# Optimization experiments

Measured on AMD Instinct MI355X. Metric: run time of the kernel, lower is better.

The kernel has to match this reference:

```python
import jax, jax.numpy as jnp
import numpy as np

N = 50000   # nodes of the target node type
E = 800000  # edges per incoming edge type (avg degree 16)
D = 128     # in == hidden == out channels (required by the module's pooling layer)


def sage_mean(x, edge_index, Wl, bl, Wr):
    """PyG SAGEConv with mean aggregation: lin_l(mean_j x_j) + lin_r(x_i).
    Note: per the original code, sources are gathered from the TARGET node
    feature table (x_input = x_dict[tgt_node_type])."""
    src, tgt = edge_index[0], edge_index[1]
    msg = x[src]                                                   # [E, D] gather
    agg = jax.ops.segment_sum(msg, tgt, num_segments=x.shape[0])   # [N, D] scatter-add
    cnt = jax.ops.segment_sum(jnp.ones((edge_index.shape[1],), x.dtype), tgt,
                              num_segments=x.shape[0])             # [N] degree
    agg = agg / jnp.maximum(cnt, 1.0)[:, None]                     # mean; 0 for isolated nodes
    return agg @ Wl + bl + x @ Wr                                  # [N, D]


def setup_inputs() -> dict:
    key = jax.random.key(0)
    ks = jax.random.split(key, 6)
    s = 1.0 / np.sqrt(D)
    x = jax.random.normal(ks[0], (N, D), jnp.float32)
    edge_index_a = jax.random.randint(ks[1], (2, E), 0, N)
    edge_index_b = jax.random.randint(ks[2], (2, E), 0, N)
    Wl = jax.random.normal(ks[3], (D, D), jnp.float32) * s
    Wr = jax.random.normal(ks[4], (D, D), jnp.float32) * s
    bl = jnp.zeros((D,), jnp.float32)
    Wp = jax.random.normal(ks[5], (D, D), jnp.float32) * s
    bp = jnp.zeros((D,), jnp.float32)
    return {"x": x, "Wl": Wl, "bl": bl, "Wr": Wr, "Wp": Wp, "bp": bp,
            "edge_index_a": edge_index_a, "edge_index_b": edge_index_b}


def reference(x, Wl, bl, Wr, Wp, bp, edge_index_a, edge_index_b):
    # One SAGEConv encoder + pooling Linear shared across incoming edge types,
    # softmax per edge type, then mean over edge types (torch.stack(...).mean(0)).
    outs = []
    for ei in (edge_index_a, edge_index_b):
        h = sage_mean(x, ei, Wl, bl, Wr)            # [N, D]
        outs.append(jax.nn.softmax(h @ Wp + bp, axis=-1))
    return (outs[0] + outs[1]) * 0.5                # [N, D]
```

## Files before the change

### kernel.cpp

```cpp
#include <hip/hip_runtime.h>
#include <math.h>

constexpr int D    = 128;
constexpr int BT   = 128;
constexpr int BTS  = 32;
constexpr int TILE = 4096;
constexpr int CE   = 128;

using bf16x8 = __attribute__((ext_vector_type(8))) short;
using f32x4  = __attribute__((ext_vector_type(4))) float;
using f32x2  = __attribute__((ext_vector_type(2))) float;
#define MFMA16 __builtin_amdgcn_mfma_f32_16x16x32_bf16

__device__ __forceinline__ unsigned short f2bf(float f) {
    unsigned u = __builtin_bit_cast(unsigned, f);
    u = (u + 0x7FFF + ((u >> 16) & 1)) >> 16;
    return (unsigned short)u;
}

__global__ __launch_bounds__(256)
void wprod_kernel(const float* __restrict__ Wl, const float* __restrict__ Wr,
                  const float* __restrict__ Wp,
                  const float* __restrict__ bl, const float* __restrict__ bp,
                  unsigned short* __restrict__ WlpB, unsigned short* __restrict__ WrpB,
                  float* __restrict__ cvec)
{
    __shared__ float wm[128 * 129];
    __shared__ float wpc[128 * 16];

    const int bid = blockIdx.x;
    const int m   = bid >> 3;
    const int cg  = bid & 7;
    const int c0  = cg * 16;
    const float* Wm = m ? Wr : Wl;
    unsigned short* OB = m ? WrpB : WlpB;
    const int t = threadIdx.x;

    for (int i = t; i < 128 * 128; i += 256) {
        int r = i >> 7, k = i & 127;
        wm[r * 129 + k] = Wm[i];
    }
    for (int i = t; i < 2048; i += 256) {
        int k = i >> 4, col = i & 15;
        wpc[i] = Wp[k * 128 + c0 + col];
    }
    __syncthreads();

    const int r = t >> 1;
    const int h = (t & 1) * 8;
    float acc[8];
    #pragma unroll
    for (int j = 0; j < 8; ++j) acc[j] = 0.f;

    for (int k = 0; k < 128; ++k) {
        float wv = wm[r * 129 + k];
        #pragma unroll
        for (int j = 0; j < 8; ++j) acc[j] += wv * wpc[k * 16 + h + j];
    }

    const int kt = r >> 5, lhi = (r >> 3) & 3, jj = r & 7;
    #pragma unroll
    for (int j = 0; j < 8; ++j) {
        int l = lhi * 16 + h + j;
        OB[((size_t)(kt * 8 + cg) * 64 + l) * 8 + jj] = f2bf(acc[j]);
    }

    if (m == 0 && t < 16) {
        int c = c0 + t;
        float s = bp[c];
        for (int k = 0; k < 128; ++k) s += bl[k] * wpc[k * 16 + t];
        cvec[c] = s;
    }
}

__global__ __launch_bounds__(256)
void prep_kernel(const int* __restrict__ ea, int Ea,
                 const int* __restrict__ eb, int Eb,
                 unsigned int* __restrict__ ent_a, int* __restrict__ cnt_a,
                 unsigned int* __restrict__ ent_b, int* __restrict__ cnt_b,
                 int NBKT, int CAP, int GA)
{
    __shared__ int hist[512];
    __shared__ int base[512];

    const int bid = blockIdx.x;
    const int t   = threadIdx.x;

    const int type = (bid >= GA);
    const int* e   = type ? eb : ea;
    const int  E   = type ? Eb : Ea;
    unsigned int* ent = type ? ent_b : ent_a;
    int* cnt          = type ? cnt_b : cnt_a;
    const int i0 = (bid - type * GA) * TILE;

    for (int h = t; h < NBKT; h += 256) hist[h] = 0;
    __syncthreads();

    int tgts[16];
    #pragma unroll
    for (int j = 0; j < 16; ++j) {
        int i = i0 + j * 256 + t;
        tgts[j] = (i < E) ? e[(size_t)E + i] : -1;
        if (tgts[j] >= 0) atomicAdd(&hist[tgts[j] >> 7], 1);
    }
    __syncthreads();

    for (int h = t; h < NBKT; h += 256) {
        base[h] = (hist[h] > 0) ? atomicAdd(&cnt[h], hist[h]) : 0;
        hist[h] = 0;
    }
    __syncthreads();

    #pragma unroll
    for (int j = 0; j < 16; ++j) {
        int i = i0 + j * 256 + t;
        if (tgts[j] >= 0) {
            int b   = tgts[j] >> 7;
            int pos = base[b] + atomicAdd(&hist[b], 1);
            if (pos < CAP)
                ent[(size_t)b * CAP + pos] = ((unsigned)e[i] << 7) | (tgts[j] & 127);
        }
    }
}

__global__ __launch_bounds__(512)
void sort_kernel(const unsigned int* __restrict__ ent_a, const int* __restrict__ cnt_a,
                 const unsigned int* __restrict__ ent_b, const int* __restrict__ cnt_b,
                 unsigned short* __restrict__ srcl_g, int* __restrict__ off_g,
                 int NBKT, int CAP)
{
    extern __shared__ __align__(16) char smem_raw[];
    int* tmp  = (int*)smem_raw;
    int* off  = tmp + CAP;
    int* cur  = off + BT + 1;
    int* wtot = cur + BT;
    unsigned short* srcl = (unsigned short*)(wtot + 2);

    const int bid  = blockIdx.x;
    const int type = (bid >= NBKT);
    const int k    = bid - type * NBKT;
    const unsigned int* ent = type ? ent_b : ent_a;
    const int cnt = min((type ? cnt_b : cnt_a)[k], CAP);

    const int t = threadIdx.x, l = t & 63, w = t >> 6;

    if (t < BT) off[t] = 0;
    __syncthreads();

    for (int i = t; i < cnt; i += 512) {
        unsigned e = ent[(size_t)k * CAP + i];
        tmp[i] = (int)e;
        atomicAdd(&off[e & (BT - 1)], 1);
    }
    __syncthreads();

    int v = 0, s = 0;
    if (t < BT) {
        v = off[t]; s = v;
        #pragma unroll
        for (int o = 1; o < 64; o <<= 1) {
            int u = __shfl_up(s, o, 64);
            if (l >= o) s += u;
        }
        if (l == 63) wtot[w] = s;
    }
    __syncthreads();
    if (t < BT) {
        int ex = ((w == 1) ? wtot[0] : 0) + s - v;
        off[t] = ex; cur[t] = ex;
    }
    if (t == 0) off[BT] = wtot[0] + wtot[1];
    __syncthreads();

    for (int i = t; i < cnt; i += 512) {
        unsigned e = (unsigned)tmp[i];
        int pos = atomicAdd(&cur[e & (BT - 1)], 1);
        srcl[pos] = (unsigned short)(e >> 7);
    }
    __syncthreads();

    for (int i = t; i < cnt; i += 512)
        srcl_g[(size_t)bid * CAP + i] = srcl[i];
    if (t <= BT)
        off_g[(size_t)bid * (BT + 1) + t] = off[t];
}

__global__ __launch_bounds__(256)
void gemmz_kernel(const float* __restrict__ x,
                  const unsigned short* __restrict__ WlpB,
                  const unsigned short* __restrict__ WrpB,
                  const float* __restrict__ cvec,
                  unsigned short* __restrict__ zl, unsigned short* __restrict__ zr,
                  int N)
{
    const int t = threadIdx.x, w = t >> 6, l = t & 63;
    const int q = l & 15, kg = l >> 4;
    const int node0 = blockIdx.x * 64 + w * 16;
    const int arow = min(node0 + q, N - 1);

    const float4* xp = reinterpret_cast<const float4*>(x + (size_t)arow * D);
    bf16x8 fx[4];
    #pragma unroll
    for (int kt = 0; kt < 4; ++kt) {
        float4 a = xp[kt * 8 + kg * 2];
        float4 b = xp[kt * 8 + kg * 2 + 1];
        bf16x8 f;
        f[0] = (short)f2bf(a.x); f[1] = (short)f2bf(a.y);
        f[2] = (short)f2bf(a.z); f[3] = (short)f2bf(a.w);
        f[4] = (short)f2bf(b.x); f[5] = (short)f2bf(b.y);
        f[6] = (short)f2bf(b.z); f[7] = (short)f2bf(b.w);
        fx[kt] = f;
    }

    #pragma unroll
    for (int nt = 0; nt < 8; ++nt) {
        f32x4 cl = {0.f, 0.f, 0.f, 0.f};
        f32x4 cr = {0.f, 0.f, 0.f, 0.f};
        #pragma unroll
        for (int kt = 0; kt < 4; ++kt) {
            const size_t fo = ((size_t)(kt * 8 + nt) * 64 + l) * 8;
            bf16x8 wl = *reinterpret_cast<const bf16x8*>(WlpB + fo);
            bf16x8 wr = *reinterpret_cast<const bf16x8*>(WrpB + fo);
            cl = MFMA16(fx[kt], wl, cl, 0, 0, 0);
            cr = MFMA16(fx[kt], wr, cr, 0, 0, 0);
        }
        float cv = cvec[nt * 16 + q];
        const int sidx = nt >> 1;
        const int cin  = (nt & 1) * 16 + q;
        #pragma unroll
        for (int r = 0; r < 4; ++r) {
            int grow = node0 + kg * 4 + r;
            if (grow < N) {
                zl[((size_t)sidx * (N + 1) + grow) * 32 + cin] = f2bf(cl[r]);
                zr[(size_t)grow * D + nt * 16 + q]             = f2bf(cr[r] + cv);
            }
        }
    }
}

__global__ __launch_bounds__(256)
void gather_kernel(const unsigned short* __restrict__ zl,
                   const unsigned short* __restrict__ srcl_g,
                   const int* __restrict__ off_g,
                   unsigned short* __restrict__ agg_a,
                   unsigned short* __restrict__ agg_b,
                   int N, int NBKT, int CAP)
{
    __shared__ int off[BTS + 1];
    __shared__ unsigned short stage[2][CE * 32];

    const int bid   = blockIdx.x;
    const int slice = bid & 3;
    const int rest  = bid >> 2;
    const int sb    = rest & 3;
    const int tb    = rest >> 2;
    const int type  = (tb >= NBKT);
    const int k     = tb - type * NBKT;

    const int t = threadIdx.x, l = t & 63, w = t >> 6;
    const int tg = l >> 3;
    const int c8 = l & 7;

    for (int i = t; i <= BTS; i += 256)
        off[i] = off_g[(size_t)tb * (BT + 1) + sb * BTS + i];
    __syncthreads();

    const int base0 = off[0];
    const int cnt   = off[BTS] - base0;
    const unsigned short* zs = zl + (size_t)slice * (N + 1) * 32;
    const unsigned short* sl = srcl_g + (size_t)tb * CAP;

    const int tt = w * 8 + tg;
    const int o0 = off[tt], o1 = off[tt + 1];
    f32x2 aP = {0.f, 0.f}, aQ = {0.f, 0.f};

    const int nc = (cnt + CE - 1) / CE;

#define STAGE(cc, bb)                                                         \
    {                                                                         \
        const int _c0 = base0 + (cc) * CE;                                    \
        _Pragma("unroll")                                                     \
        for (int i = 0; i < 2; ++i) {                                         \
            const int el = w * 32 + i * 16 + (l >> 2);                        \
            const unsigned sid = sl[_c0 + el];                                \
            const char* g = (const char*)zs + (size_t)sid * 64 + (l & 3) * 16;\
            char* ldsb = (char*)stage[bb] + (size_t)(w * 32 + i * 16) * 64;   \
            __builtin_amdgcn_global_load_lds(                                 \
                (const __attribute__((address_space(1))) unsigned*)g,         \
                (__attribute__((address_space(3))) unsigned*)ldsb, 16, 0, 0); \
        }                                                                     \
    }

    if (nc > 0) STAGE(0, 0);

    for (int c = 0; c < nc; ++c) {
        if (c + 1 < nc) {
            STAGE(c + 1, (c + 1) & 1);
            asm volatile("s_waitcnt vmcnt(2)" ::: "memory");
        } else {
            asm volatile("s_waitcnt vmcnt(0)" ::: "memory");
        }
        __builtin_amdgcn_s_barrier();
        asm volatile("" ::: "memory");

        const int c0 = base0 + c * CE;
        const unsigned short* sg = stage[c & 1];
        const int lo = max(o0, c0);
        const int hi = min(o1, c0 + CE);
        int j = lo;
        for (; j + 1 < hi; j += 2) {
            uint2 v0 = *reinterpret_cast<const uint2*>(sg + (j - c0) * 32 + c8 * 4);
            uint2 v1 = *reinterpret_cast<const uint2*>(sg + (j + 1 - c0) * 32 + c8 * 4);
            f32x2 p0, q0, p1, q1;
            p0[0] = __builtin_bit_cast(float, v0.x << 16);
            p0[1] = __builtin_bit_cast(float, v0.y << 16);
            q0[0] = __builtin_bit_cast(float, v0.x & 0xffff0000u);
            q0[1] = __builtin_bit_cast(float, v0.y & 0xffff0000u);
            p1[0] = __builtin_bit_cast(float, v1.x << 16);
            p1[1] = __builtin_bit_cast(float, v1.y << 16);
            q1[0] = __builtin_bit_cast(float, v1.x & 0xffff0000u);
            q1[1] = __builtin_bit_cast(float, v1.y & 0xffff0000u);
            aP += p0 + p1;
            aQ += q0 + q1;
        }
        if (j < hi) {
            uint2 v0 = *reinterpret_cast<const uint2*>(sg + (j - c0) * 32 + c8 * 4);
            f32x2 p0, q0;
            p0[0] = __builtin_bit_cast(float, v0.x << 16);
            p0[1] = __builtin_bit_cast(float, v0.y << 16);
            q0[0] = __builtin_bit_cast(float, v0.x & 0xffff0000u);
            q0[1] = __builtin_bit_cast(float, v0.y & 0xffff0000u);
            aP += p0;
            aQ += q0;
        }
        asm volatile("" ::: "memory");
        __builtin_amdgcn_s_barrier();
    }
#undef STAGE

    unsigned short* agg = (type ? agg_b : agg_a) + (size_t)slice * N * 32;
    const int n = k * BT + sb * BTS + tt;
    const int deg = o1 - o0;
    if (n < N) {
        const float r = 1.0f / fmaxf((float)deg, 1.0f);
        uint2 o;
        o.x = ((unsigned)f2bf(aQ[0] * r) << 16) | f2bf(aP[0] * r);
        o.y = ((unsigned)f2bf(aQ[1] * r) << 16) | f2bf(aP[1] * r);
        *reinterpret_cast<uint2*>(agg + (size_t)n * 32 + c8 * 4) = o;
    }
}

__global__ __launch_bounds__(256)
void epi_kernel(const unsigned short* __restrict__ agg_a,
                const unsigned short* __restrict__ agg_b,
                const unsigned short* __restrict__ zr,
                float* __restrict__ out, int N)
{
    const int t = threadIdx.x;
    const int n = blockIdx.x * 16 + (t >> 4);
    const int c = t & 15;
    if (n >= N) return;

    const int s = c >> 2;
    const size_t aoff = ((size_t)s * N + n) * 32 + (c & 3) * 8;
    uint4 va = *reinterpret_cast<const uint4*>(agg_a + aoff);
    uint4 vb = *reinterpret_cast<const uint4*>(agg_b + aoff);
    uint4 vz = *reinterpret_cast<const uint4*>(zr + (size_t)n * D + c * 8);

    unsigned ua[4] = {va.x, va.y, va.z, va.w};
    unsigned ub[4] = {vb.x, vb.y, vb.z, vb.w};
    unsigned uz[4] = {vz.x, vz.y, vz.z, vz.w};

    float la[8], lb[8];
    #pragma unroll
    for (int d = 0; d < 4; ++d) {
        float z0 = __builtin_bit_cast(float, uz[d] << 16);
        float z1 = __builtin_bit_cast(float, uz[d] & 0xffff0000u);
        la[2*d]   = __builtin_bit_cast(float, ua[d] << 16) + z0;
        la[2*d+1] = __builtin_bit_cast(float, ua[d] & 0xffff0000u) + z1;
        lb[2*d]   = __builtin_bit_cast(float, ub[d] << 16) + z0;
        lb[2*d+1] = __builtin_bit_cast(float, ub[d] & 0xffff0000u) + z1;
    }

    float ma = -INFINITY, mb = -INFINITY;
    #pragma unroll
    for (int j = 0; j < 8; ++j) { ma = fmaxf(ma, la[j]); mb = fmaxf(mb, lb[j]); }
    #pragma unroll
    for (int o = 1; o < 16; o <<= 1) {
        ma = fmaxf(ma, __shfl_xor(ma, o, 64));
        mb = fmaxf(mb, __shfl_xor(mb, o, 64));
    }
    float sa = 0.f, sb = 0.f;
    #pragma unroll
    for (int j = 0; j < 8; ++j) {
        la[j] = __expf(la[j] - ma); sa += la[j];
        lb[j] = __expf(lb[j] - mb); sb += lb[j];
    }
    #pragma unroll
    for (int o = 1; o < 16; o <<= 1) {
        sa += __shfl_xor(sa, o, 64);
        sb += __shfl_xor(sb, o, 64);
    }
    const float ra = 0.5f / sa, rb = 0.5f / sb;

    float4 o0, o1;
    o0.x = la[0]*ra + lb[0]*rb; o0.y = la[1]*ra + lb[1]*rb;
    o0.z = la[2]*ra + lb[2]*rb; o0.w = la[3]*ra + lb[3]*rb;
    o1.x = la[4]*ra + lb[4]*rb; o1.y = la[5]*ra + lb[5]*rb;
    o1.z = la[6]*ra + lb[6]*rb; o1.w = la[7]*ra + lb[7]*rb;
    float* op = out + (size_t)n * D + c * 8;
    *reinterpret_cast<float4*>(op)     = o0;
    *reinterpret_cast<float4*>(op + 4) = o1;
}

extern "C" void kernel_launch(void* const* d_in, const int* in_sizes, int n_in,
                              void* d_out, int out_size, void* d_ws, size_t ws_size,
                              hipStream_t stream)
{
    const float* x  = (const float*)d_in[0];
    const float* Wl = (const float*)d_in[1];
    const float* bl = (const float*)d_in[2];
    const float* Wr = (const float*)d_in[3];
    const float* Wp = (const float*)d_in[4];
    const float* bp = (const float*)d_in[5];
    const int*   ea = (const int*)d_in[6];
    const int*   eb = (const int*)d_in[7];

    const int N  = in_sizes[0] / D;
    const int Ea = in_sizes[6] / 2;
    const int Eb = in_sizes[7] / 2;

    const int NBKT = (N + BT - 1) / BT;
    const int Emax = Ea > Eb ? Ea : Eb;
    int CAP = (int)(((long long)Emax * BT / N) * 5 / 4 + 128);
    CAP = (CAP + 7) & ~7;

    unsigned int* ent_a = (unsigned int*)d_ws;
    unsigned int* ent_b = ent_a + (size_t)NBKT * CAP;
    int* cnt_a = (int*)(ent_b + (size_t)NBKT * CAP);
    int* cnt_b = cnt_a + NBKT;
    int* off_g = cnt_b + NBKT;
    float* cvec = (float*)(off_g + (size_t)2 * NBKT * (BT + 1));
    uintptr_t p = (uintptr_t)(cvec + 128);
    p = (p + 15) & ~(uintptr_t)15;
    unsigned short* srcl_g = (unsigned short*)p;
    unsigned short* zl     = srcl_g + (size_t)2 * NBKT * CAP + 512;
    unsigned short* zr     = zl + (size_t)4 * (N + 1) * 32;
    unsigned short* agg_a  = zr + (size_t)N * D;
    unsigned short* agg_b  = agg_a + (size_t)N * D;
    unsigned short* WlpB   = agg_b + (size_t)N * D;
    unsigned short* WrpB   = WlpB + D * D;

    hipMemsetAsync(cnt_a, 0, sizeof(int) * 2 * (size_t)NBKT, stream);

    wprod_kernel<<<16, 256, 0, stream>>>(Wl, Wr, Wp, bl, bp, WlpB, WrpB, cvec);

    const int GA = (Ea + TILE - 1) / TILE;
    const int GB = (Eb + TILE - 1) / TILE;
    prep_kernel<<<GA + GB, 256, 0, stream>>>(ea, Ea, eb, Eb,
                                             ent_a, cnt_a, ent_b, cnt_b,
                                             NBKT, CAP, GA);

    const int smem_sort = CAP * 6 + (BT + 1 + BT + 2) * 4 + 16;
    sort_kernel<<<2 * NBKT, 512, smem_sort, stream>>>(
        ent_a, cnt_a, ent_b, cnt_b, srcl_g, off_g, NBKT, CAP);

    gemmz_kernel<<<(N + 63) / 64, 256, 0, stream>>>(
        x, WlpB, WrpB, cvec, zl, zr, N);

    gather_kernel<<<2 * NBKT * 4 * 4, 256, 0, stream>>>(
        zl, srcl_g, off_g, agg_a, agg_b, N, NBKT, CAP);

    epi_kernel<<<(N + 15) / 16, 256, 0, stream>>>(agg_a, agg_b, zr,
                                                  (float*)d_out, N);
}
```

Before: 140.6 us.

## Merge weight-product with edge bucketing, sort with node GEMM, single-stage gather

Weight-product blocks now run in the same launch as the edge bucketing, and the bucket sort shares a launch with the node GEMM (now 512 threads, 128 nodes per block). This removes two kernel launches and lets independent work overlap. The gather kernel drops its double-buffered 128-edge chunking and instead stages up to 576 rows into one larger LDS buffer per pass, then waits once. That cuts barriers for typical bucket sizes but loses the load/compute overlap and enlarges LDS use, which may lower occupancy. The sort kernel's dynamic shared memory size now also applies to the GEMM blocks.

```diff
diff --git a/kernel.cpp b/kernel.cpp
--- a/kernel.cpp
+++ b/kernel.cpp
@@ -5,7 +5,7 @@
 constexpr int BT   = 128;
 constexpr int BTS  = 32;
 constexpr int TILE = 4096;
-constexpr int CE   = 128;
+constexpr int SCAP = 576;
 
 using bf16x8 = __attribute__((ext_vector_type(8))) short;
 using f32x4  = __attribute__((ext_vector_type(4))) float;
@@ -19,220 +19,218 @@
 }
 
 __global__ __launch_bounds__(256)
-void wprod_kernel(const float* __restrict__ Wl, const float* __restrict__ Wr,
+void prepA_kernel(const float* __restrict__ Wl, const float* __restrict__ Wr,
                   const float* __restrict__ Wp,
                   const float* __restrict__ bl, const float* __restrict__ bp,
                   unsigned short* __restrict__ WlpB, unsigned short* __restrict__ WrpB,
-                  float* __restrict__ cvec)
+                  float* __restrict__ cvec,
+                  const int* __restrict__ ea, int Ea,
+                  const int* __restrict__ eb, int Eb,
+                  unsigned int* __restrict__ ent_a, int* __restrict__ cnt_a,
+                  unsigned int* __restrict__ ent_b, int* __restrict__ cnt_b,
+                  int NBKT, int CAP, int GA)
 {
     __shared__ float wm[128 * 129];
     __shared__ float wpc[128 * 16];
-
-    const int bid = blockIdx.x;
-    const int m   = bid >> 3;
-    const int cg  = bid & 7;
-    const int c0  = cg * 16;
-    const float* Wm = m ? Wr : Wl;
-    unsigned short* OB = m ? WrpB : WlpB;
-    const int t = threadIdx.x;
-
-    for (int i = t; i < 128 * 128; i += 256) {
-        int r = i >> 7, k = i & 127;
-        wm[r * 129 + k] = Wm[i];
-    }
-    for (int i = t; i < 2048; i += 256) {
-        int k = i >> 4, col = i & 15;
-        wpc[i] = Wp[k * 128 + c0 + col];
-    }
-    __syncthreads();
-
-    const int r = t >> 1;
-    const int h = (t & 1) * 8;
-    float acc[8];
-    #pragma unroll
-    for (int j = 0; j < 8; ++j) acc[j] = 0.f;
-
-    for (int k = 0; k < 128; ++k) {
-        float wv = wm[r * 129 + k];
-        #pragma unroll
-        for (int j = 0; j < 8; ++j) acc[j] += wv * wpc[k * 16 + h + j];
-    }
-
-    const int kt = r >> 5, lhi = (r >> 3) & 3, jj = r & 7;
-    #pragma unroll
-    for (int j = 0; j < 8; ++j) {
-        int l = lhi * 16 + h + j;
-        OB[((size_t)(kt * 8 + cg) * 64 + l) * 8 + jj] = f2bf(acc[j]);
-    }
-
-    if (m == 0 && t < 16) {
-        int c = c0 + t;
-        float s = bp[c];
-        for (int k = 0; k < 128; ++k) s += bl[k] * wpc[k * 16 + t];
-        cvec[c] = s;
-    }
-}
-
-__global__ __launch_bounds__(256)
-void prep_kernel(const int* __restrict__ ea, int Ea,
-                 const int* __restrict__ eb, int Eb,
-                 unsigned int* __restrict__ ent_a, int* __restrict__ cnt_a,
-                 unsigned int* __restrict__ ent_b, int* __restrict__ cnt_b,
-                 int NBKT, int CAP, int GA)
-{
     __shared__ int hist[512];
     __shared__ int base[512];
 
     const int bid = blockIdx.x;
     const int t   = threadIdx.x;
 
-    const int type = (bid >= GA);
-    const int* e   = type ? eb : ea;
-    const int  E   = type ? Eb : Ea;
-    unsigned int* ent = type ? ent_b : ent_a;
-    int* cnt          = type ? cnt_b : cnt_a;
-    const int i0 = (bid - type * GA) * TILE;
-
-    for (int h = t; h < NBKT; h += 256) hist[h] = 0;
-    __syncthreads();
-
-    int tgts[16];
-    #pragma unroll
-    for (int j = 0; j < 16; ++j) {
-        int i = i0 + j * 256 + t;
-        tgts[j] = (i < E) ? e[(size_t)E + i] : -1;
-        if (tgts[j] >= 0) atomicAdd(&hist[tgts[j] >> 7], 1);
-    }
-    __syncthreads();
-
-    for (int h = t; h < NBKT; h += 256) {
-        base[h] = (hist[h] > 0) ? atomicAdd(&cnt[h], hist[h]) : 0;
-        hist[h] = 0;
-    }
-    __syncthreads();
-
-    #pragma unroll
-    for (int j = 0; j < 16; ++j) {
-        int i = i0 + j * 256 + t;
-        if (tgts[j] >= 0) {
-            int b   = tgts[j] >> 7;
-            int pos = base[b] + atomicAdd(&hist[b], 1);
-            if (pos < CAP)
-                ent[(size_t)b * CAP + pos] = ((unsigned)e[i] << 7) | (tgts[j] & 127);
+    if (bid < 16) {
+        const int m   = bid >> 3;
+        const int cg  = bid & 7;
+        const int c0  = cg * 16;
+        const float* Wm = m ? Wr : Wl;
+        unsigned short* OB = m ? WrpB : WlpB;
+
+        for (int i = t; i < 128 * 128; i += 256) {
+            int r = i >> 7, k = i & 127;
+            wm[r * 129 + k] = Wm[i];
+        }
+        for (int i = t; i < 2048; i += 256) {
+            int k = i >> 4, col = i & 15;
+            wpc[i] = Wp[k * 128 + c0 + col];
+        }
+        __syncthreads();
+
+        const int r = t >> 1;
+        const int h = (t & 1) * 8;
+        float acc[8];
+        #pragma unroll
+        for (int j = 0; j < 8; ++j) acc[j] = 0.f;
+
+        for (int k = 0; k < 128; ++k) {
+            float wv = wm[r * 129 + k];
+            #pragma unroll
+            for (int j = 0; j < 8; ++j) acc[j] += wv * wpc[k * 16 + h + j];
+        }
+
+        const int kt = r >> 5, lhi = (r >> 3) & 3, jj = r & 7;
+        #pragma unroll
+        for (int j = 0; j < 8; ++j) {
+            int l = lhi * 16 + h + j;
+            OB[((size_t)(kt * 8 + cg) * 64 + l) * 8 + jj] = f2bf(acc[j]);
+        }
+
+        if (m == 0 && t < 16) {
+            int c = c0 + t;
+            float s = bp[c];
+            for (int k = 0; k < 128; ++k) s += bl[k] * wpc[k * 16 + t];
+            cvec[c] = s;
+        }
+    } else {
+        const int pb   = bid - 16;
+        const int type = (pb >= GA);
+        const int* e   = type ? eb : ea;
+        const int  E   = type ? Eb : Ea;
+        unsigned int* ent = type ? ent_b : ent_a;
+        int* cnt          = type ? cnt_b : cnt_a;
+        const int i0 = (pb - type * GA) * TILE;
+
+        for (int h = t; h < NBKT; h += 256) hist[h] = 0;
+        __syncthreads();
+
+        int tgts[16];
+        #pragma unroll
+        for (int j = 0; j < 16; ++j) {
+            int i = i0 + j * 256 + t;
+            tgts[j] = (i < E) ? e[(size_t)E + i] : -1;
+            if (tgts[j] >= 0) atomicAdd(&hist[tgts[j] >> 7], 1);
+        }
+        __syncthreads();
+
+        for (int h = t; h < NBKT; h += 256) {
+            base[h] = (hist[h] > 0) ? atomicAdd(&cnt[h], hist[h]) : 0;
+            hist[h] = 0;
+        }
+        __syncthreads();
+
+        #pragma unroll
+        for (int j = 0; j < 16; ++j) {
+            int i = i0 + j * 256 + t;
+            if (tgts[j] >= 0) {
+                int b   = tgts[j] >> 7;
+                int pos = base[b] + atomicAdd(&hist[b], 1);
+                if (pos < CAP)
+                    ent[(size_t)b * CAP + pos] = ((unsigned)e[i] << 7) | (tgts[j] & 127);
+            }
         }
     }
 }
 
 __global__ __launch_bounds__(512)
-void sort_kernel(const unsigned int* __restrict__ ent_a, const int* __restrict__ cnt_a,
-                 const unsigned int* __restrict__ ent_b, const int* __restrict__ cnt_b,
-                 unsigned short* __restrict__ srcl_g, int* __restrict__ off_g,
-                 int NBKT, int CAP)
-{
-    extern __shared__ __align__(16) char smem_raw[];
-    int* tmp  = (int*)smem_raw;
-    int* off  = tmp + CAP;
-    int* cur  = off + BT + 1;
-    int* wtot = cur + BT;
-    unsigned short* srcl = (unsigned short*)(wtot + 2);
-
-    const int bid  = blockIdx.x;
-    const int type = (bid >= NBKT);
-    const int k    = bid - type * NBKT;
-    const unsigned int* ent = type ? ent_b : ent_a;
-    const int cnt = min((type ? cnt_b : cnt_a)[k], CAP);
-
-    const int t = threadIdx.x, l = t & 63, w = t >> 6;
-
-    if (t < BT) off[t] = 0;
-    __syncthreads();
-
-    for (int i = t; i < cnt; i += 512) {
-        unsigned e = ent[(size_t)k * CAP + i];
-        tmp[i] = (int)e;
-        atomicAdd(&off[e & (BT - 1)], 1);
-    }
-    __syncthreads();
-
-    int v = 0, s = 0;
-    if (t < BT) {
-        v = off[t]; s = v;
-        #pragma unroll
-        for (int o = 1; o < 64; o <<= 1) {
-            int u = __shfl_up(s, o, 64);
-            if (l >= o) s += u;
-        }
-        if (l == 63) wtot[w] = s;
-    }
-    __syncthreads();
-    if (t < BT) {
-        int ex = ((w == 1) ? wtot[0] : 0) + s - v;
-        off[t] = ex; cur[t] = ex;
-    }
-    if (t == 0) off[BT] = wtot[0] + wtot[1];
-    __syncthreads();
-
-    for (int i = t; i < cnt; i += 512) {
-        unsigned e = (unsigned)tmp[i];
-        int pos = atomicAdd(&cur[e & (BT - 1)], 1);
-        srcl[pos] = (unsigned short)(e >> 7);
-    }
-    __syncthreads();
-
-    for (int i = t; i < cnt; i += 512)
-        srcl_g[(size_t)bid * CAP + i] = srcl[i];
-    if (t <= BT)
-        off_g[(size_t)bid * (BT + 1) + t] = off[t];
-}
-
-__global__ __launch_bounds__(256)
-void gemmz_kernel(const float* __restrict__ x,
+void sortB_kernel(const unsigned int* __restrict__ ent_a, const int* __restrict__ cnt_a,
+                  const unsigned int* __restrict__ ent_b, const int* __restrict__ cnt_b,
+                  unsigned short* __restrict__ srcl_g, int* __restrict__ off_g,
+                  const float* __restrict__ x,
                   const unsigned short* __restrict__ WlpB,
                   const unsigned short* __restrict__ WrpB,
                   const float* __restrict__ cvec,
                   unsigned short* __restrict__ zl, unsigned short* __restrict__ zr,
-                  int N)
+                  int N, int NBKT, int CAP)
 {
-    const int t = threadIdx.x, w = t >> 6, l = t & 63;
-    const int q = l & 15, kg = l >> 4;
-    const int node0 = blockIdx.x * 64 + w * 16;
-    const int arow = min(node0 + q, N - 1);
-
-    const float4* xp = reinterpret_cast<const float4*>(x + (size_t)arow * D);
-    bf16x8 fx[4];
-    #pragma unroll
-    for (int kt = 0; kt < 4; ++kt) {
-        float4 a = xp[kt * 8 + kg * 2];
-        float4 b = xp[kt * 8 + kg * 2 + 1];
-        bf16x8 f;
-        f[0] = (short)f2bf(a.x); f[1] = (short)f2bf(a.y);
-        f[2] = (short)f2bf(a.z); f[3] = (short)f2bf(a.w);
-        f[4] = (short)f2bf(b.x); f[5] = (short)f2bf(b.y);
-        f[6] = (short)f2bf(b.z); f[7] = (short)f2bf(b.w);
-        fx[kt] = f;
-    }
-
-    #pragma unroll
-    for (int nt = 0; nt < 8; ++nt) {
-        f32x4 cl = {0.f, 0.f, 0.f, 0.f};
-        f32x4 cr = {0.f, 0.f, 0.f, 0.f};
+    extern __shared__ __align__(16) char smem_raw[];
+
+    const int bid = blockIdx.x;
+    const int t   = threadIdx.x;
+
+    if (bid < 2 * NBKT) {
+        int* tmp  = (int*)smem_raw;
+        int* off  = tmp + CAP;
+        int* cur  = off + BT + 1;
+        int* wtot = cur + BT;
+        unsigned short* srcl = (unsigned short*)(wtot + 2);
+
+        const int type = (bid >= NBKT);
+        const int k    = bid - type * NBKT;
+        const unsigned int* ent = type ? ent_b : ent_a;
+        const int cnt = min((type ? cnt_b : cnt_a)[k], CAP);
+        const int l = t & 63, w = t >> 6;
+
+        if (t < BT) off[t] = 0;
+        __syncthreads();
+
+        for (int i = t; i < cnt; i += 512) {
+            unsigned e = ent[(size_t)k * CAP + i];
+            tmp[i] = (int)e;
+            atomicAdd(&off[e & (BT - 1)], 1);
+        }
+        __syncthreads();
+
+        int v = 0, s = 0;
+        if (t < BT) {
+            v = off[t]; s = v;
+            #pragma unroll
+            for (int o = 1; o < 64; o <<= 1) {
+                int u = __shfl_up(s, o, 64);
+                if (l >= o) s += u;
+            }
+            if (l == 63) wtot[w] = s;
+        }
+        __syncthreads();
+        if (t < BT) {
+            int ex = ((w == 1) ? wtot[0] : 0) + s - v;
+            off[t] = ex; cur[t] = ex;
+        }
+        if (t == 0) off[BT] = wtot[0] + wtot[1];
+        __syncthreads();
+
+        for (int i = t; i < cnt; i += 512) {
+            unsigned e = (unsigned)tmp[i];
+            int pos = atomicAdd(&cur[e & (BT - 1)], 1);
+            srcl[pos] = (unsigned short)(e >> 7);
+        }
+        __syncthreads();
+
+        for (int i = t; i < cnt; i += 512)
+            srcl_g[(size_t)bid * CAP + i] = srcl[i];
+        if (t <= BT)
+            off_g[(size_t)bid * (BT + 1) + t] = off[t];
+    } else {
+        const int gb = bid - 2 * NBKT;
+        const int w = t >> 6, l = t & 63;
+        const int q = l & 15, kg = l >> 4;
+        const int node0 = gb * 128 + w * 16;
+        const int arow = min(node0 + q, N - 1);
+
+        const float4* xp = reinterpret_cast<const float4*>(x + (size_t)arow * D);
+        bf16x8 fx[4];
         #pragma unroll
         for (int kt = 0; kt < 4; ++kt) {
-            const size_t fo = ((size_t)(kt * 8 + nt) * 64 + l) * 8;
-            bf16x8 wl = *reinterpret_cast<const bf16x8*>(WlpB + fo);
-            bf16x8 wr = *reinterpret_cast<const bf16x8*>(WrpB + fo);
-            cl = MFMA16(fx[kt], wl, cl, 0, 0, 0);
-            cr = MFMA16(fx[kt], wr, cr, 0, 0, 0);
-        }
-        float cv = cvec[nt * 16 + q];
-        const int sidx = nt >> 1;
-        const int cin  = (nt & 1) * 16 + q;
-        #pragma unroll
-        for (int r = 0; r < 4; ++r) {
-            int grow = node0 + kg * 4 + r;
-            if (grow < N) {
-                zl[((size_t)sidx * (N + 1) + grow) * 32 + cin] = f2bf(cl[r]);
-                zr[(size_t)grow * D + nt * 16 + q]             = f2bf(cr[r] + cv);
+            float4 a = xp[kt * 8 + kg * 2];
+            float4 b = xp[kt * 8 + kg * 2 + 1];
+            bf16x8 f;
+            f[0] = (short)f2bf(a.x); f[1] = (short)f2bf(a.y);
+            f[2] = (short)f2bf(a.z); f[3] = (short)f2bf(a.w);
+            f[4] = (short)f2bf(b.x); f[5] = (short)f2bf(b.y);
+            f[6] = (short)f2bf(b.z); f[7] = (short)f2bf(b.w);
+            fx[kt] = f;
+        }
+
+        #pragma unroll
+        for (int nt = 0; nt < 8; ++nt) {
+            f32x4 cl = {0.f, 0.f, 0.f, 0.f};
+            f32x4 cr = {0.f, 0.f, 0.f, 0.f};
+            #pragma unroll
+            for (int kt = 0; kt < 4; ++kt) {
+                const size_t fo = ((size_t)(kt * 8 + nt) * 64 + l) * 8;
+                bf16x8 wl = *reinterpret_cast<const bf16x8*>(WlpB + fo);
+                bf16x8 wr = *reinterpret_cast<const bf16x8*>(WrpB + fo);
+                cl = MFMA16(fx[kt], wl, cl, 0, 0, 0);
+                cr = MFMA16(fx[kt], wr, cr, 0, 0, 0);
+            }
+            float cv = cvec[nt * 16 + q];
+            const int sidx = nt >> 1;
+            const int cin  = (nt & 1) * 16 + q;
+            #pragma unroll
+            for (int r = 0; r < 4; ++r) {
+                int grow = node0 + kg * 4 + r;
+                if (grow < N) {
+                    zl[((size_t)sidx * (N + 1) + grow) * 32 + cin] = f2bf(cl[r]);
+                    zr[(size_t)grow * D + nt * 16 + q]             = f2bf(cr[r] + cv);
+                }
             }
         }
     }
@@ -247,7 +245,7 @@
                    int N, int NBKT, int CAP)
 {
     __shared__ int off[BTS + 1];
-    __shared__ unsigned short stage[2][CE * 32];
+    __shared__ __align__(16) unsigned short stage[SCAP * 32];
 
     const int bid   = blockIdx.x;
     const int slice = bid & 3;
@@ -274,69 +272,57 @@
     const int o0 = off[tt], o1 = off[tt + 1];
     f32x2 aP = {0.f, 0.f}, aQ = {0.f, 0.f};
 
-    const int nc = (cnt + CE - 1) / CE;
-
-#define STAGE(cc, bb)                                                         \
-    {                                                                         \
-        const int _c0 = base0 + (cc) * CE;                                    \
-        _Pragma("unroll")                                                     \
-        for (int i = 0; i < 2; ++i) {                                         \
-            const int el = w * 32 + i * 16 + (l >> 2);                        \
-            const unsigned sid = sl[_c0 + el];                                \
-            const char* g = (const char*)zs + (size_t)sid * 64 + (l & 3) * 16;\
-            char* ldsb = (char*)stage[bb] + (size_t)(w * 32 + i * 16) * 64;   \
-            __builtin_amdgcn_global_load_lds(                                 \
-                (const __attribute__((address_space(1))) unsigned*)g,         \
-                (__attribute__((address_space(3))) unsigned*)ldsb, 16, 0, 0); \
-        }                                                                     \
-    }
-
-    if (nc > 0) STAGE(0, 0);
-
-    for (int c = 0; c < nc; ++c) {
-        if (c + 1 < nc) {
-            STAGE(c + 1, (c + 1) & 1);
-            asm volatile("s_waitcnt vmcnt(2)" ::: "memory");
-        } else {
-            asm volatile("s_waitcnt vmcnt(0)" ::: "memory");
-        }
+    for (int p0 = 0; p0 < cnt; p0 += SCAP) {
+        const int c0 = base0 + p0;
+        const int ce = min(cnt - p0, SCAP);
+
+        #pragma unroll
+        for (int i = 0; i < SCAP / 64; ++i) {
+            const int e0 = (i * 4 + w) * 16;
+            if (e0 < ce) {
+                const int el = e0 + (l >> 2);
+                const unsigned sid = sl[c0 + el];
+                const char* g = (const char*)zs + (size_t)sid * 64 + (l & 3) * 16;
+                char* ldsb = (char*)stage + (size_t)e0 * 64;
+                __builtin_amdgcn_global_load_lds(
+                    (const __attribute__((address_space(1))) unsigned*)g,
+                    (__attribute__((address_space(3))) unsigned*)ldsb, 16, 0, 0);
+            }
+        }
+        asm volatile("s_waitcnt vmcnt(0)" ::: "memory");
         __builtin_amdgcn_s_barrier();
         asm volatile("" ::: "memory");
 
-        const int c0 = base0 + c * CE;
-        const unsigned short* sg = stage[c & 1];
         const int lo = max(o0, c0);
-        const int hi = min(o1, c0 + CE);
+        const int hi = min(o1, c0 + ce);
         int j = lo;
         for (; j + 1 < hi; j += 2) {
-            uint2 v0 = *reinterpret_cast<const uint2*>(sg + (j - c0) * 32 + c8 * 4);
-            uint2 v1 = *reinterpret_cast<const uint2*>(sg + (j + 1 - c0) * 32 + c8 * 4);
-            f32x2 p0, q0, p1, q1;
-            p0[0] = __builtin_bit_cast(float, v0.x << 16);
-            p0[1] = __builtin_bit_cast(float, v0.y << 16);
-            q0[0] = __builtin_bit_cast(float, v0.x & 0xffff0000u);
-            q0[1] = __builtin_bit_cast(float, v0.y & 0xffff0000u);
-            p1[0] = __builtin_bit_cast(float, v1.x << 16);
-            p1[1] = __builtin_bit_cast(float, v1.y << 16);
-            q1[0] = __builtin_bit_cast(float, v1.x & 0xffff0000u);
-            q1[1] = __builtin_bit_cast(float, v1.y & 0xffff0000u);
-            aP += p0 + p1;
-            aQ += q0 + q1;
+            uint2 v0 = *reinterpret_cast<const uint2*>(stage + (j - c0) * 32 + c8 * 4);
+            uint2 v1 = *reinterpret_cast<const uint2*>(stage + (j + 1 - c0) * 32 + c8 * 4);
+            f32x2 p0v, q0v, p1v, q1v;
+            p0v[0] = __builtin_bit_cast(float, v0.x << 16);
+            p0v[1] = __builtin_bit_cast(float, v0.y << 16);
+            q0v[0] = __builtin_bit_cast(float, v0.x & 0xffff0000u);
+            q0v[1] = __builtin_bit_cast(float, v0.y & 0xffff0000u);
+            p1v[0] = __builtin_bit_cast(float, v1.x << 16);
+            p1v[1] = __builtin_bit_cast(float, v1.y << 16);
+            q1v[0] = __builtin_bit_cast(float, v1.x & 0xffff0000u);
+            q1v[1] = __builtin_bit_cast(float, v1.y & 0xffff0000u);
+            aP += p0v + p1v;
+            aQ += q0v + q1v;
         }
         if (j < hi) {
-            uint2 v0 = *reinterpret_cast<const uint2*>(sg + (j - c0) * 32 + c8 * 4);
-            f32x2 p0, q0;
-            p0[0] = __builtin_bit_cast(float, v0.x << 16);
-            p0[1] = __builtin_bit_cast(float, v0.y << 16);
-            q0[0] = __builtin_bit_cast(float, v0.x & 0xffff0000u);
-            q0[1] = __builtin_bit_cast(float, v0.y & 0xffff0000u);
-            aP += p0;
-            aQ += q0;
-        }
-        asm volatile("" ::: "memory");
-        __builtin_amdgcn_s_barrier();
-    }
-#undef STAGE
+            uint2 v0 = *reinterpret_cast<const uint2*>(stage + (j - c0) * 32 + c8 * 4);
+            f32x2 p0v, q0v;
+            p0v[0] = __builtin_bit_cast(float, v0.x << 16);
+            p0v[1] = __builtin_bit_cast(float, v0.y << 16);
+            q0v[0] = __builtin_bit_cast(float, v0.x & 0xffff0000u);
+            q0v[1] = __builtin_bit_cast(float, v0.y & 0xffff0000u);
+            aP += p0v;
+            aQ += q0v;
+        }
+        if (p0 + SCAP < cnt) __syncthreads();
+    }
 
     unsigned short* agg = (type ? agg_b : agg_a) + (size_t)slice * N * 32;
     const int n = k * BT + sb * BTS + tt;
@@ -444,7 +430,7 @@
     uintptr_t p = (uintptr_t)(cvec + 128);
     p = (p + 15) & ~(uintptr_t)15;
     unsigned short* srcl_g = (unsigned short*)p;
-    unsigned short* zl     = srcl_g + (size_t)2 * NBKT * CAP + 512;
+    unsigned short* zl     = srcl_g + (size_t)2 * NBKT * CAP + 1024;
     unsigned short* zr     = zl + (size_t)4 * (N + 1) * 32;
     unsigned short* agg_a  = zr + (size_t)N * D;
     unsigned short* agg_b  = agg_a + (size_t)N * D;
@@ -453,20 +439,18 @@
 
     hipMemsetAsync(cnt_a, 0, sizeof(int) * 2 * (size_t)NBKT, stream);
 
-    wprod_kernel<<<16, 256, 0, stream>>>(Wl, Wr, Wp, bl, bp, WlpB, WrpB, cvec);
-
     const int GA = (Ea + TILE - 1) / TILE;
     const int GB = (Eb + TILE - 1) / TILE;
-    prep_kernel<<<GA + GB, 256, 0, stream>>>(ea, Ea, eb, Eb,
-                                             ent_a, cnt_a, ent_b, cnt_b,
-                                             NBKT, CAP, GA);
-
+
+    prepA_kernel<<<16 + GA + GB, 256, 0, stream>>>(
+        Wl, Wr, Wp, bl, bp, WlpB, WrpB, cvec,
+        ea, Ea, eb, Eb, ent_a, cnt_a, ent_b, cnt_b, NBKT, CAP, GA);
+
+    const int GZ = (N + 127) / 128;
     const int smem_sort = CAP * 6 + (BT + 1 + BT + 2) * 4 + 16;
-    sort_kernel<<<2 * NBKT, 512, smem_sort, stream>>>(
-        ent_a, cnt_a, ent_b, cnt_b, srcl_g, off_g, NBKT, CAP);
-
-    gemmz_kernel<<<(N + 63) / 64, 256, 0, stream>>>(
-        x, WlpB, WrpB, cvec, zl, zr, N);
+    sortB_kernel<<<2 * NBKT + GZ, 512, smem_sort, stream>>>(
+        ent_a, cnt_a, ent_b, cnt_b, srcl_g, off_g,
+        x, WlpB, WrpB, cvec, zl, zr, N, NBKT, CAP);
 
     gather_kernel<<<2 * NBKT * 4 * 4, 256, 0, stream>>>(
         zl, srcl_g, off_g, agg_a, agg_b, N, NBKT, CAP);
```

New measurement: 140.9 us. No clear change (+0.2%).
